# Optimization experiments

Measured on AMD Instinct MI355X. Metric: run time of the kernel, lower is better.

## Reference

```python
import jax, jax.numpy as jnp
import numpy as np

B, D = 8192, 128
TEMP = 0.07
EPS = 1e-12  # F.normalize default eps (clamp on norm)


def _l2norm(x):
    n = jnp.sqrt(jnp.sum(x * x, axis=1, keepdims=True))
    return x / jnp.maximum(n, EPS)


def setup_inputs() -> dict:
    key = jax.random.key(0)
    k1, k2, k3, k4 = jax.random.split(key, 4)
    return {
        "feat_fv": jax.random.normal(k1, (B, D), dtype=jnp.float32),
        "feat_fi": jax.random.normal(k2, (B, D), dtype=jnp.float32),
        "feat_v": jax.random.normal(k3, (B, D), dtype=jnp.float32),
        "feat_i": jax.random.normal(k4, (B, D), dtype=jnp.float32),
    }


def reference(feat_fv, feat_fi, feat_v, feat_i):
    fv = _l2norm(feat_fv)
    fi = _l2norm(feat_fi)
    v = _l2norm(feat_v)
    vi = _l2norm(feat_i)

    # positive logits: per-sample dot products [B]
    pos_v = jnp.sum(fv * v, axis=1)
    pos_i = jnp.sum(fi * vi, axis=1)
    use_v = pos_v >= pos_i                      # branch condition per row
    pos = jnp.where(use_v, pos_v, pos_i)        # [B]

    # full pairwise dot products, branch-select per row
    Sv = jnp.einsum('bd,kd->bk', fv, v)         # [B, B]
    Si = jnp.einsum('bd,kd->bk', fi, vi)        # [B, B]
    S = jnp.where(use_v[:, None], Sv, Si)       # [B, B]

    n = S.shape[0]
    diag = jnp.eye(n, dtype=bool)
    # negatives exclude the positive (diagonal) entry -> mask to -inf
    neg_logits = jnp.where(diag, -jnp.inf, S / TEMP)  # [B, B]

    # cross-entropy with target class 0 (the positive), reduction='none':
    # loss_b = logsumexp([pos/T, negs/T]) - pos/T
    lse = jnp.logaddexp(pos / TEMP, jax.scipy.special.logsumexp(neg_logits, axis=1))
    return lse - pos / TEMP
```

## Files before the change

### kernel.cpp

```cpp
#include <hip/hip_runtime.h>
#include <math.h>

#define Bsz 8192
#define Dd  128
#define BM  64
#define NSLICE 8
#define ROT2(x) ((((x) << 2) | ((x) >> 4)) & 63)

typedef __attribute__((ext_vector_type(8))) short short8;
typedef __attribute__((ext_vector_type(4))) float float4v;

static constexpr float INV_T = 1.0f / 0.07f;
static constexpr float K1 =  20.60992915555662f;
static constexpr float K2 = -20.60992915555662f;

static __device__ inline unsigned pack_bf16(float x, float y) {
    union { float f; unsigned u; } a, b;
    a.f = x; b.f = y;
    unsigned ra = a.u + 0x7FFF + ((a.u >> 16) & 1);
    unsigned rb = b.u + 0x7FFF + ((b.u >> 16) & 1);
    return (ra >> 16) | (rb & 0xFFFF0000u);
}

__global__ void init_kernel(unsigned long long* __restrict__ cnt) {
    if (threadIdx.x == 0) cnt[0] = 0ull;
}

__global__ __launch_bounds__(1024) void prep_kernel(
    const float4* __restrict__ fv4, const float4* __restrict__ fi4,
    const float4* __restrict__ v4,  const float4* __restrict__ vi4,
    unsigned* __restrict__ Xb, uint2* __restrict__ Yf0, uint2* __restrict__ Yf1,
    float* __restrict__ posArr, int* __restrict__ origArr, int* __restrict__ flagArr,
    float* __restrict__ lAcc, unsigned long long* __restrict__ cnt)
{
    __shared__ unsigned sT0[32 * 66];
    __shared__ unsigned sT1[32 * 66];
    __shared__ int sFlagL[32];
    __shared__ int sRank[32];
    __shared__ unsigned sBase[2];

    const int t    = threadIdx.x;
    const int wave = t >> 6;
    const int lane = t & 63;
    const int half = lane >> 5;
    const int c    = lane & 31;
    const int rl   = wave * 2 + half;
    const int b    = blockIdx.x * 32 + rl;
    const int src  = b * 32 + c;

    const float4 afv = fv4[src];
    const float4 afi = fi4[src];
    const float4 av  = v4[src];
    const float4 avi = vi4[src];

    float nfv = afv.x*afv.x + afv.y*afv.y + afv.z*afv.z + afv.w*afv.w;
    float nfi = afi.x*afi.x + afi.y*afi.y + afi.z*afi.z + afi.w*afi.w;
    float nv  = av.x*av.x   + av.y*av.y   + av.z*av.z   + av.w*av.w;
    float nvi = avi.x*avi.x + avi.y*avi.y + avi.z*avi.z + avi.w*avi.w;
    float dv  = afv.x*av.x  + afv.y*av.y  + afv.z*av.z  + afv.w*av.w;
    float di  = afi.x*avi.x + afi.y*avi.y + afi.z*avi.z + afi.w*avi.w;

    #pragma unroll
    for (int m = 1; m < 32; m <<= 1) {
        nfv += __shfl_xor(nfv, m);
        nfi += __shfl_xor(nfi, m);
        nv  += __shfl_xor(nv,  m);
        nvi += __shfl_xor(nvi, m);
        dv  += __shfl_xor(dv,  m);
        di  += __shfl_xor(di,  m);
    }

    const float rnfv = 1.0f / fmaxf(sqrtf(nfv), 1e-12f);
    const float rnfi = 1.0f / fmaxf(sqrtf(nfi), 1e-12f);
    const float rnv  = 1.0f / fmaxf(sqrtf(nv ), 1e-12f);
    const float rnvi = 1.0f / fmaxf(sqrtf(nvi), 1e-12f);

    const float pos_v = dv * rnfv * rnv;
    const float pos_i = di * rnfi * rnvi;
    const bool useV = (pos_v >= pos_i);
    const float pos = useV ? pos_v : pos_i;

    uint2 w0y = make_uint2(pack_bf16(av.x  * rnv,  av.y  * rnv),
                           pack_bf16(av.z  * rnv,  av.w  * rnv));
    uint2 w1y = make_uint2(pack_bf16(avi.x * rnvi, avi.y * rnvi),
                           pack_bf16(avi.z * rnvi, avi.w * rnvi));
    *(uint2*)&sT0[rl * 66 + c * 2] = w0y;
    *(uint2*)&sT1[rl * 66 + c * 2] = w1y;
    if (c == 0) sFlagL[rl] = useV ? 0 : 1;
    __syncthreads();

    if (t < 64) {
        const int f = (lane < 32) ? sFlagL[lane] : 2;
        const unsigned long long m0 = __ballot(f == 0);
        const unsigned long long m1 = __ballot(f == 1);
        if (lane == 0) {
            const unsigned long long add =
                (unsigned long long)__popcll(m0) | ((unsigned long long)__popcll(m1) << 32);
            const unsigned long long ret = atomicAdd(cnt, add);
            sBase[0] = (unsigned)(ret & 0xffffffffull);
            sBase[1] = (unsigned)(ret >> 32);
        }
        if (lane < 32) {
            const unsigned long long below = (1ull << lane) - 1ull;
            sRank[lane] = (f == 0) ? (int)__popcll(m0 & below) : (int)__popcll(m1 & below);
        }
    }

    {
        const int tl = t >> 9;
        const int kc = (t >> 7) & 3;
        const int lp = (t >> 1) & 63;
        const int w0 = (t & 1) * 2;
        const int row = tl * 16 + (lp & 15);
        const int s   = kc * 16 + (lp >> 4) * 4 + w0;
        Yf0[blockIdx.x * 1024 + t] = *(const uint2*)&sT0[row * 66 + s];
        Yf1[blockIdx.x * 1024 + t] = *(const uint2*)&sT1[row * 66 + s];
    }
    __syncthreads();

    const int f  = sFlagL[rl];
    const int rk = sRank[rl];
    const int p  = (f == 0) ? (int)(sBase[0] + rk) : (Bsz - 1 - (int)(sBase[1] + rk));

    const float sc = useV ? rnfv : rnfi;
    const float x0 = useV ? afv.x : afi.x;
    const float x1 = useV ? afv.y : afi.y;
    const float x2 = useV ? afv.z : afi.z;
    const float x3 = useV ? afv.w : afi.w;
    ((uint2*)Xb)[p * 32 + c] = make_uint2(pack_bf16(x0 * sc, x1 * sc),
                                          pack_bf16(x2 * sc, x3 * sc));

    if (c == 0) {
        posArr[p]  = pos;
        origArr[p] = b;
        flagArr[p] = f;
        lAcc[p]    = 0.0f;
    }
}

__global__ __launch_bounds__(256, 4) void main_kernel(
    const unsigned short* __restrict__ Xb,
    const uint4* __restrict__ Yf0q, const uint4* __restrict__ Yf1q,
    const int* __restrict__ flagArr, float* __restrict__ lAcc)
{
    __shared__ uint4 sXf[1024];
    __shared__ int sFlag[BM];
    __shared__ int sHas[2];

    const int t    = threadIdx.x;
    const int wave = t >> 6;
    const int lane = t & 63;
    const int quad = lane >> 4;
    const int mrow = lane & 15;
    const int slice = blockIdx.x & 7;
    const int p0    = (blockIdx.x >> 3) * BM;

    if (t < 2) sHas[t] = 0;
    __syncthreads();
    if (t < BM) {
        const int f = flagArr[p0 + t];
        sFlag[t] = f;
        atomicOr(&sHas[f], 1);
    }

    #pragma unroll
    for (int it = 0; it < 4; ++it) {
        const int i = t + it * 256;
        const int row = i >> 4, ch = i & 15;
        const uint4 val = ((const uint4*)Xb)[(p0 + row) * 16 + ch];
        const int blk16 = (row >> 4) * 4 + (ch >> 2);
        const int slot  = (ch & 3) * 16 + (row & 15);
        sXf[blk16 * 64 + ROT2(slot)] = val;
    }
    __syncthreads();

    short8 afr[4][4];
    #pragma unroll
    for (int rt = 0; rt < 4; ++rt)
        #pragma unroll
        for (int kc = 0; kc < 4; ++kc)
            afr[rt][kc] = *(const short8*)&sXf[(rt * 4 + kc) * 64 + ROT2(lane)];

    const int g0 = slice * 64 + wave * 16;

    for (int phase = 0; phase < 2; ++phase) {
        if (!sHas[phase]) continue;
        const uint4* __restrict__ yb = (phase ? Yf1q : Yf0q) + (size_t)g0 * 256 + lane;

        float rowsum[4][4] = {};

        short8 b0 = *(const short8*)&yb[0];
        short8 b1 = *(const short8*)&yb[64];
        short8 b2 = *(const short8*)&yb[128];
        short8 b3 = *(const short8*)&yb[192];

        #pragma unroll 1
        for (int jt = 0; jt < 16; ++jt) {
            float4v acc[4] = {};
            #pragma unroll
            for (int rt = 0; rt < 4; ++rt)
                acc[rt] = __builtin_amdgcn_mfma_f32_16x16x32_bf16(afr[rt][0], b0, acc[rt], 0, 0, 0);
            #pragma unroll
            for (int rt = 0; rt < 4; ++rt)
                acc[rt] = __builtin_amdgcn_mfma_f32_16x16x32_bf16(afr[rt][1], b1, acc[rt], 0, 0, 0);
            if (jt < 15) {
                b0 = *(const short8*)&yb[256];
                b1 = *(const short8*)&yb[320];
            }
            #pragma unroll
            for (int rt = 0; rt < 4; ++rt)
                acc[rt] = __builtin_amdgcn_mfma_f32_16x16x32_bf16(afr[rt][2], b2, acc[rt], 0, 0, 0);
            #pragma unroll
            for (int rt = 0; rt < 4; ++rt)
                acc[rt] = __builtin_amdgcn_mfma_f32_16x16x32_bf16(afr[rt][3], b3, acc[rt], 0, 0, 0);
            if (jt < 15) {
                b2 = *(const short8*)&yb[384];
                b3 = *(const short8*)&yb[448];
            }
            yb += 256;

            #pragma unroll
            for (int rt = 0; rt < 4; ++rt)
                #pragma unroll
                for (int r = 0; r < 4; ++r)
                    rowsum[rt][r] += exp2f(fmaf(acc[rt][r], K1, K2));
        }

        #pragma unroll
        for (int m = 1; m < 16; m <<= 1)
            #pragma unroll
            for (int rt = 0; rt < 4; ++rt)
                #pragma unroll
                for (int r = 0; r < 4; ++r)
                    rowsum[rt][r] += __shfl_xor(rowsum[rt][r], m);

        if (mrow == 0) {
            #pragma unroll
            for (int rt = 0; rt < 4; ++rt)
                #pragma unroll
                for (int r = 0; r < 4; ++r) {
                    const int row = rt * 16 + quad * 4 + r;
                    if (sFlag[row] == phase)
                        atomicAdd(&lAcc[p0 + row], rowsum[rt][r]);
                }
        }
    }
}

__global__ __launch_bounds__(256) void finish_kernel(
    const float* __restrict__ lAcc, const float* __restrict__ posArr,
    const int* __restrict__ origArr, float* __restrict__ out)
{
    const int p = blockIdx.x * 256 + threadIdx.x;
    out[origArr[p]] = logf(lAcc[p]) + INV_T - posArr[p] * INV_T;
}

extern "C" void kernel_launch(void* const* d_in, const int* in_sizes, int n_in,
                              void* d_out, int out_size, void* d_ws, size_t ws_size,
                              hipStream_t stream)
{
    const float4* fv = (const float4*)d_in[0];
    const float4* fi = (const float4*)d_in[1];
    const float4* v  = (const float4*)d_in[2];
    const float4* vi = (const float4*)d_in[3];
    float* out = (float*)d_out;

    unsigned short* Xb  = (unsigned short*)d_ws;
    unsigned short* Yf0 = Xb  + Bsz * Dd;
    unsigned short* Yf1 = Yf0 + Bsz * Dd;
    float* posArr = (float*)(Yf1 + Bsz * Dd);
    float* lAcc   = posArr + Bsz;
    int*  origArr = (int*)(lAcc + Bsz);
    int*  flagArr = origArr + Bsz;
    unsigned long long* cnt = (unsigned long long*)(flagArr + Bsz);

    hipLaunchKernelGGL(init_kernel, dim3(1), dim3(64), 0, stream, cnt);
    hipLaunchKernelGGL(prep_kernel, dim3(Bsz / 32), dim3(1024), 0, stream,
                       fv, fi, v, vi, (unsigned*)Xb, (uint2*)Yf0, (uint2*)Yf1,
                       posArr, origArr, flagArr, lAcc, cnt);
    hipLaunchKernelGGL(main_kernel, dim3((Bsz / BM) * NSLICE), dim3(256), 0, stream,
                       Xb, (const uint4*)Yf0, (const uint4*)Yf1, flagArr, lAcc);
    hipLaunchKernelGGL(finish_kernel, dim3(Bsz / 256), dim3(256), 0, stream,
                       lAcc, posArr, origArr, out);
}
```

Measured before the change: 110.2 us.

## Fuse finish into main kernel via fixed-point counted atomics; double-buffer B loads

```diff
diff --git a/kernel.cpp b/kernel.cpp
--- a/kernel.cpp
+++ b/kernel.cpp
@@ -13,6 +13,11 @@
 static constexpr float INV_T = 1.0f / 0.07f;
 static constexpr float K1 =  20.60992915555662f;
 static constexpr float K2 = -20.60992915555662f;
+static constexpr float SCALE     = 1099511627776.0f;
+static constexpr float INV_SCALE = 1.0f / 1099511627776.0f;
+#define CNT_SHIFT 55
+#define NCONTRIB  (NSLICE * 4)
+#define SUM_MASK  ((1ULL << CNT_SHIFT) - 1ULL)
 
 static __device__ inline unsigned pack_bf16(float x, float y) {
     union { float f; unsigned u; } a, b;
@@ -31,7 +36,7 @@
     const float4* __restrict__ v4,  const float4* __restrict__ vi4,
     unsigned* __restrict__ Xb, uint2* __restrict__ Yf0, uint2* __restrict__ Yf1,
     float* __restrict__ posArr, int* __restrict__ origArr, int* __restrict__ flagArr,
-    float* __restrict__ lAcc, unsigned long long* __restrict__ cnt)
+    unsigned long long* __restrict__ lAcc64, unsigned long long* __restrict__ cnt)
 {
     __shared__ unsigned sT0[32 * 66];
     __shared__ unsigned sT1[32 * 66];
@@ -134,14 +139,16 @@
         posArr[p]  = pos;
         origArr[p] = b;
         flagArr[p] = f;
-        lAcc[p]    = 0.0f;
-    }
-}
-
-__global__ __launch_bounds__(256, 4) void main_kernel(
+        lAcc64[p]  = 0ull;
+    }
+}
+
+__global__ __launch_bounds__(256, 3) void main_kernel(
     const unsigned short* __restrict__ Xb,
     const uint4* __restrict__ Yf0q, const uint4* __restrict__ Yf1q,
-    const int* __restrict__ flagArr, float* __restrict__ lAcc)
+    const int* __restrict__ flagArr, unsigned long long* __restrict__ lAcc64,
+    const float* __restrict__ posArr, const int* __restrict__ origArr,
+    float* __restrict__ out)
 {
     __shared__ uint4 sXf[1024];
     __shared__ int sFlag[BM];
@@ -183,47 +190,58 @@
 
     const int g0 = slice * 64 + wave * 16;
 
+#define COMPUTE_TILE(B0, B1, B2, B3)                                              \
+    do {                                                                          \
+        float4v acc[4] = {};                                                      \
+        _Pragma("unroll")                                                         \
+        for (int rt = 0; rt < 4; ++rt)                                            \
+            acc[rt] = __builtin_amdgcn_mfma_f32_16x16x32_bf16(afr[rt][0], B0, acc[rt], 0, 0, 0); \
+        _Pragma("unroll")                                                         \
+        for (int rt = 0; rt < 4; ++rt)                                            \
+            acc[rt] = __builtin_amdgcn_mfma_f32_16x16x32_bf16(afr[rt][1], B1, acc[rt], 0, 0, 0); \
+        _Pragma("unroll")                                                         \
+        for (int rt = 0; rt < 4; ++rt)                                            \
+            acc[rt] = __builtin_amdgcn_mfma_f32_16x16x32_bf16(afr[rt][2], B2, acc[rt], 0, 0, 0); \
+        _Pragma("unroll")                                                         \
+        for (int rt = 0; rt < 4; ++rt)                                            \
+            acc[rt] = __builtin_amdgcn_mfma_f32_16x16x32_bf16(afr[rt][3], B3, acc[rt], 0, 0, 0); \
+        _Pragma("unroll")                                                         \
+        for (int rt = 0; rt < 4; ++rt)                                            \
+            _Pragma("unroll")                                                     \
+            for (int r = 0; r < 4; ++r)                                           \
+                rowsum[rt][r] += exp2f(fmaf(acc[rt][r], K1, K2));                 \
+    } while (0)
+
     for (int phase = 0; phase < 2; ++phase) {
         if (!sHas[phase]) continue;
         const uint4* __restrict__ yb = (phase ? Yf1q : Yf0q) + (size_t)g0 * 256 + lane;
 
         float rowsum[4][4] = {};
 
-        short8 b0 = *(const short8*)&yb[0];
-        short8 b1 = *(const short8*)&yb[64];
-        short8 b2 = *(const short8*)&yb[128];
-        short8 b3 = *(const short8*)&yb[192];
+        short8 bA0 = *(const short8*)&yb[0];
+        short8 bA1 = *(const short8*)&yb[64];
+        short8 bA2 = *(const short8*)&yb[128];
+        short8 bA3 = *(const short8*)&yb[192];
 
         #pragma unroll 1
-        for (int jt = 0; jt < 16; ++jt) {
-            float4v acc[4] = {};
-            #pragma unroll
-            for (int rt = 0; rt < 4; ++rt)
-                acc[rt] = __builtin_amdgcn_mfma_f32_16x16x32_bf16(afr[rt][0], b0, acc[rt], 0, 0, 0);
-            #pragma unroll
-            for (int rt = 0; rt < 4; ++rt)
-                acc[rt] = __builtin_amdgcn_mfma_f32_16x16x32_bf16(afr[rt][1], b1, acc[rt], 0, 0, 0);
-            if (jt < 15) {
-                b0 = *(const short8*)&yb[256];
-                b1 = *(const short8*)&yb[320];
+        for (int p8 = 0; p8 < 8; ++p8) {
+            const uint4* __restrict__ y0 = yb + p8 * 512;
+
+            short8 bB0 = *(const short8*)&y0[256];
+            short8 bB1 = *(const short8*)&y0[320];
+            short8 bB2 = *(const short8*)&y0[384];
+            short8 bB3 = *(const short8*)&y0[448];
+
+            COMPUTE_TILE(bA0, bA1, bA2, bA3);
+
+            if (p8 < 7) {
+                bA0 = *(const short8*)&y0[512];
+                bA1 = *(const short8*)&y0[576];
+                bA2 = *(const short8*)&y0[640];
+                bA3 = *(const short8*)&y0[704];
             }
-            #pragma unroll
-            for (int rt = 0; rt < 4; ++rt)
-                acc[rt] = __builtin_amdgcn_mfma_f32_16x16x32_bf16(afr[rt][2], b2, acc[rt], 0, 0, 0);
-            #pragma unroll
-            for (int rt = 0; rt < 4; ++rt)
-                acc[rt] = __builtin_amdgcn_mfma_f32_16x16x32_bf16(afr[rt][3], b3, acc[rt], 0, 0, 0);
-            if (jt < 15) {
-                b2 = *(const short8*)&yb[384];
-                b3 = *(const short8*)&yb[448];
-            }
-            yb += 256;
-
-            #pragma unroll
-            for (int rt = 0; rt < 4; ++rt)
-                #pragma unroll
-                for (int r = 0; r < 4; ++r)
-                    rowsum[rt][r] += exp2f(fmaf(acc[rt][r], K1, K2));
+
+            COMPUTE_TILE(bB0, bB1, bB2, bB3);
         }
 
         #pragma unroll
@@ -240,19 +258,23 @@
                 #pragma unroll
                 for (int r = 0; r < 4; ++r) {
                     const int row = rt * 16 + quad * 4 + r;
-                    if (sFlag[row] == phase)
-                        atomicAdd(&lAcc[p0 + row], rowsum[rt][r]);
+                    if (sFlag[row] == phase) {
+                        const unsigned long long add =
+                            (unsigned long long)(rowsum[rt][r] * SCALE)
+                            | (1ULL << CNT_SHIFT);
+                        const unsigned long long ret =
+                            atomicAdd(&lAcc64[p0 + row], add);
+                        if ((ret >> CNT_SHIFT) == NCONTRIB - 1) {
+                            const unsigned long long tot = (ret + add) & SUM_MASK;
+                            const float s = (float)tot * INV_SCALE;
+                            out[origArr[p0 + row]] =
+                                logf(s) + INV_T - posArr[p0 + row] * INV_T;
+                        }
+                    }
                 }
         }
     }
-}
-
-__global__ __launch_bounds__(256) void finish_kernel(
-    const float* __restrict__ lAcc, const float* __restrict__ posArr,
-    const int* __restrict__ origArr, float* __restrict__ out)
-{
-    const int p = blockIdx.x * 256 + threadIdx.x;
-    out[origArr[p]] = logf(lAcc[p]) + INV_T - posArr[p] * INV_T;
+#undef COMPUTE_TILE
 }
 
 extern "C" void kernel_launch(void* const* d_in, const int* in_sizes, int n_in,
@@ -269,17 +291,17 @@
     unsigned short* Yf0 = Xb  + Bsz * Dd;
     unsigned short* Yf1 = Yf0 + Bsz * Dd;
     float* posArr = (float*)(Yf1 + Bsz * Dd);
-    float* lAcc   = posArr + Bsz;
-    int*  origArr = (int*)(lAcc + Bsz);
+    unsigned long long* lAcc64 =
+        (unsigned long long*)(posArr + Bsz);
+    int*  origArr = (int*)(lAcc64 + Bsz);
     int*  flagArr = origArr + Bsz;
     unsigned long long* cnt = (unsigned long long*)(flagArr + Bsz);
 
     hipLaunchKernelGGL(init_kernel, dim3(1), dim3(64), 0, stream, cnt);
     hipLaunchKernelGGL(prep_kernel, dim3(Bsz / 32), dim3(1024), 0, stream,
                        fv, fi, v, vi, (unsigned*)Xb, (uint2*)Yf0, (uint2*)Yf1,
-                       posArr, origArr, flagArr, lAcc, cnt);
+                       posArr, origArr, flagArr, lAcc64, cnt);
     hipLaunchKernelGGL(main_kernel, dim3((Bsz / BM) * NSLICE), dim3(256), 0, stream,
-                       Xb, (const uint4*)Yf0, (const uint4*)Yf1, flagArr, lAcc);
-    hipLaunchKernelGGL(finish_kernel, dim3(Bsz / 256), dim3(256), 0, stream,
-                       lAcc, posArr, origArr, out);
-}
+                       Xb, (const uint4*)Yf0, (const uint4*)Yf1, flagArr, lAcc64,
+                       posArr, origArr, out);
+}
```

Result: slower. 117.9 us (+7.0%).

## Fuse finish into main kernel via fixed-point counted 64-bit atomics; double slices

Applied to the files above, without the earlier changes.

```diff
diff --git a/kernel.cpp b/kernel.cpp
--- a/kernel.cpp
+++ b/kernel.cpp
@@ -4,7 +4,8 @@
 #define Bsz 8192
 #define Dd  128
 #define BM  64
-#define NSLICE 8
+#define NSLICE 16
+#define NTILE  (512 / NSLICE / 4)
 #define ROT2(x) ((((x) << 2) | ((x) >> 4)) & 63)
 
 typedef __attribute__((ext_vector_type(8))) short short8;
@@ -13,6 +14,11 @@
 static constexpr float INV_T = 1.0f / 0.07f;
 static constexpr float K1 =  20.60992915555662f;
 static constexpr float K2 = -20.60992915555662f;
+static constexpr float SCALE     = 1099511627776.0f;
+static constexpr float INV_SCALE = 1.0f / 1099511627776.0f;
+#define CNT_SHIFT 55
+#define NCONTRIB  (NSLICE * 4)
+#define SUM_MASK  ((1ULL << CNT_SHIFT) - 1ULL)
 
 static __device__ inline unsigned pack_bf16(float x, float y) {
     union { float f; unsigned u; } a, b;
@@ -31,7 +37,7 @@
     const float4* __restrict__ v4,  const float4* __restrict__ vi4,
     unsigned* __restrict__ Xb, uint2* __restrict__ Yf0, uint2* __restrict__ Yf1,
     float* __restrict__ posArr, int* __restrict__ origArr, int* __restrict__ flagArr,
-    float* __restrict__ lAcc, unsigned long long* __restrict__ cnt)
+    unsigned long long* __restrict__ lAcc64, unsigned long long* __restrict__ cnt)
 {
     __shared__ unsigned sT0[32 * 66];
     __shared__ unsigned sT1[32 * 66];
@@ -134,14 +140,16 @@
         posArr[p]  = pos;
         origArr[p] = b;
         flagArr[p] = f;
-        lAcc[p]    = 0.0f;
+        lAcc64[p]  = 0ull;
     }
 }
 
 __global__ __launch_bounds__(256, 4) void main_kernel(
     const unsigned short* __restrict__ Xb,
     const uint4* __restrict__ Yf0q, const uint4* __restrict__ Yf1q,
-    const int* __restrict__ flagArr, float* __restrict__ lAcc)
+    const int* __restrict__ flagArr, unsigned long long* __restrict__ lAcc64,
+    const float* __restrict__ posArr, const int* __restrict__ origArr,
+    float* __restrict__ out)
 {
     __shared__ uint4 sXf[1024];
     __shared__ int sFlag[BM];
@@ -152,8 +160,8 @@
     const int lane = t & 63;
     const int quad = lane >> 4;
     const int mrow = lane & 15;
-    const int slice = blockIdx.x & 7;
-    const int p0    = (blockIdx.x >> 3) * BM;
+    const int slice = blockIdx.x & (NSLICE - 1);
+    const int p0    = (blockIdx.x >> 4) * BM;
 
     if (t < 2) sHas[t] = 0;
     __syncthreads();
@@ -181,7 +189,7 @@
         for (int kc = 0; kc < 4; ++kc)
             afr[rt][kc] = *(const short8*)&sXf[(rt * 4 + kc) * 64 + ROT2(lane)];
 
-    const int g0 = slice * 64 + wave * 16;
+    const int g0 = slice * (NTILE * 4) + wave * NTILE;
 
     for (int phase = 0; phase < 2; ++phase) {
         if (!sHas[phase]) continue;
@@ -195,7 +203,7 @@
         short8 b3 = *(const short8*)&yb[192];
 
         #pragma unroll 1
-        for (int jt = 0; jt < 16; ++jt) {
+        for (int jt = 0; jt < NTILE; ++jt) {
             float4v acc[4] = {};
             #pragma unroll
             for (int rt = 0; rt < 4; ++rt)
@@ -203,7 +211,7 @@
             #pragma unroll
             for (int rt = 0; rt < 4; ++rt)
                 acc[rt] = __builtin_amdgcn_mfma_f32_16x16x32_bf16(afr[rt][1], b1, acc[rt], 0, 0, 0);
-            if (jt < 15) {
+            if (jt < NTILE - 1) {
                 b0 = *(const short8*)&yb[256];
                 b1 = *(const short8*)&yb[320];
             }
@@ -213,7 +221,7 @@
             #pragma unroll
             for (int rt = 0; rt < 4; ++rt)
                 acc[rt] = __builtin_amdgcn_mfma_f32_16x16x32_bf16(afr[rt][3], b3, acc[rt], 0, 0, 0);
-            if (jt < 15) {
+            if (jt < NTILE - 1) {
                 b2 = *(const short8*)&yb[384];
                 b3 = *(const short8*)&yb[448];
             }
@@ -240,19 +248,22 @@
                 #pragma unroll
                 for (int r = 0; r < 4; ++r) {
                     const int row = rt * 16 + quad * 4 + r;
-                    if (sFlag[row] == phase)
-                        atomicAdd(&lAcc[p0 + row], rowsum[rt][r]);
+                    if (sFlag[row] == phase) {
+                        const unsigned long long add =
+                            (unsigned long long)(rowsum[rt][r] * SCALE)
+                            | (1ULL << CNT_SHIFT);
+                        const unsigned long long ret =
+                            atomicAdd(&lAcc64[p0 + row], add);
+                        if ((ret >> CNT_SHIFT) == NCONTRIB - 1) {
+                            const unsigned long long tot = (ret + add) & SUM_MASK;
+                            const float s = (float)tot * INV_SCALE;
+                            out[origArr[p0 + row]] =
+                                logf(s) + INV_T - posArr[p0 + row] * INV_T;
+                        }
+                    }
                 }
         }
     }
-}
-
-__global__ __launch_bounds__(256) void finish_kernel(
-    const float* __restrict__ lAcc, const float* __restrict__ posArr,
-    const int* __restrict__ origArr, float* __restrict__ out)
-{
-    const int p = blockIdx.x * 256 + threadIdx.x;
-    out[origArr[p]] = logf(lAcc[p]) + INV_T - posArr[p] * INV_T;
 }
 
 extern "C" void kernel_launch(void* const* d_in, const int* in_sizes, int n_in,
@@ -269,17 +280,17 @@
     unsigned short* Yf0 = Xb  + Bsz * Dd;
     unsigned short* Yf1 = Yf0 + Bsz * Dd;
     float* posArr = (float*)(Yf1 + Bsz * Dd);
-    float* lAcc   = posArr + Bsz;
-    int*  origArr = (int*)(lAcc + Bsz);
+    unsigned long long* lAcc64 =
+        (unsigned long long*)(posArr + Bsz);
+    int*  origArr = (int*)(lAcc64 + Bsz);
     int*  flagArr = origArr + Bsz;
     unsigned long long* cnt = (unsigned long long*)(flagArr + Bsz);
 
     hipLaunchKernelGGL(init_kernel, dim3(1), dim3(64), 0, stream, cnt);
     hipLaunchKernelGGL(prep_kernel, dim3(Bsz / 32), dim3(1024), 0, stream,
                        fv, fi, v, vi, (unsigned*)Xb, (uint2*)Yf0, (uint2*)Yf1,
-                       posArr, origArr, flagArr, lAcc, cnt);
+                       posArr, origArr, flagArr, lAcc64, cnt);
     hipLaunchKernelGGL(main_kernel, dim3((Bsz / BM) * NSLICE), dim3(256), 0, stream,
-                       Xb, (const uint4*)Yf0, (const uint4*)Yf1, flagArr, lAcc);
-    hipLaunchKernelGGL(finish_kernel, dim3(Bsz / 256), dim3(256), 0, stream,
-                       lAcc, posArr, origArr, out);
-}
+                       Xb, (const uint4*)Yf0, (const uint4*)Yf1, flagArr, lAcc64,
+                       posArr, origArr, out);
+}
```

Measured after the change: 130.9 us. +18.7%, slower.
